# Kernel optimization log

Hardware: AMD Instinct MI355X
Metric: run time of the kernel (lower is better)

Reference implementation:

```python
import jax, jax.numpy as jnp
import numpy as np

B, N, DIM = 64, 197, 768        # batch, tokens (14*14 + cls), model dim
H, KD, D = 12, 64, 128          # heads, key_dim, v head dim (attn_ratio=2)
DH = H * D                      # 1536
HQKV = DH + 2 * H * KD          # 3072
EPS = 1e-5
SCALE = KD ** -0.5


def _bn(y, g, b):
    # BatchNorm1d in training mode over flattened (B*N, F): biased variance
    m = y.mean(axis=(0, 1))
    v = jnp.mean((y - m) ** 2, axis=(0, 1))
    return (y - m) * (g / jnp.sqrt(v + EPS)) + b


def setup_inputs() -> dict:
    key = jax.random.key(0)
    ks = jax.random.split(key, 7)
    return {
        "x": jax.random.normal(ks[0], (B, N, DIM), jnp.float32),
        "qkv_w": jax.random.normal(ks[1], (HQKV, DIM), jnp.float32) * 0.02,
        "qkv_g": 1.0 + 0.1 * jax.random.normal(ks[2], (HQKV,), jnp.float32),
        "qkv_b": 0.1 * jax.random.normal(ks[3], (HQKV,), jnp.float32),
        "proj_w": jax.random.normal(ks[4], (DIM, DH), jnp.float32) * 0.02,
        "proj_g": 1.0 + 0.1 * jax.random.normal(ks[5], (DIM,), jnp.float32),
        "proj_b": 0.1 * jax.random.normal(ks[6], (DIM,), jnp.float32),
    }


def reference(x, qkv_w, qkv_g, qkv_b, proj_w, proj_g, proj_b):
    # QKV projection: bias-free linear + train-mode BatchNorm1d
    qkv = _bn(jnp.einsum('bnc,fc->bnf', x, qkv_w), qkv_g, qkv_b)
    qkv = qkv.reshape(B, N, H, 2 * KD + D)
    q = qkv[..., :KD].transpose(0, 2, 1, 3)          # [B,H,N,KD]
    k = qkv[..., KD:2 * KD].transpose(0, 2, 1, 3)    # [B,H,N,KD]
    v = qkv[..., 2 * KD:].transpose(0, 2, 1, 3)      # [B,H,N,D]

    attn = jax.nn.softmax(jnp.einsum('bhqd,bhkd->bhqk', q, k) * SCALE, axis=-1)
    # auxiliary reduction: per-head-mean of cls-token row (global_attn update)
    cls_attn = attn[:, :, 0, 1:].mean(axis=1)        # [B, N-1]

    out = jnp.einsum('bhqk,bhkd->bhqd', attn, v)
    out = out.transpose(0, 2, 1, 3).reshape(B, N, DH)
    # proj: Hardswish activation, then linear + train-mode BatchNorm1d
    y = _bn(jnp.einsum('bnd,cd->bnc', jax.nn.hard_swish(out), proj_w), proj_g, proj_b)
    return y, cls_attn
```

## Files before the change

kernel.cpp:

```cpp
#include <hip/hip_runtime.h>
#include <hip/hip_bf16.h>

typedef __hip_bfloat16 bf16;
typedef __attribute__((ext_vector_type(4))) float f32x4;
typedef __attribute__((ext_vector_type(8))) short s16x8;
typedef __attribute__((ext_vector_type(4))) unsigned short u16x4;

#define NB 64
#define NT 197
#define DIM 768
#define NH 12
#define HQKV 3072
#define DH 1536
#define DV 128
#define MREAL (NB*NT)
#define MPAD 12800
#define KPAD 224
#define PSTR 232
#define CNT ((float)MREAL)

__device__ __forceinline__ float bf2f(bf16 v) { return __bfloat162float(v); }
__device__ __forceinline__ bf16  f2bf(float v){ return __float2bfloat16(v); }
__device__ __forceinline__ unsigned short f2bfu(float v){ return __builtin_bit_cast(unsigned short, __float2bfloat16(v)); }
__device__ __forceinline__ float u2f(unsigned short u){ return __builtin_bit_cast(float, (unsigned)u << 16); }

__device__ __forceinline__ void async16(const bf16* g, bf16* l) {
  __builtin_amdgcn_global_load_lds((const __attribute__((address_space(1))) void*)g,
                                   (__attribute__((address_space(3))) void*)l, 16, 0, 0);
}

__global__ void prep_kernel(const float* __restrict__ x, const float* __restrict__ qkv_w,
                            const float* __restrict__ proj_w,
                            bf16* __restrict__ xb, bf16* __restrict__ wqkvb,
                            bf16* __restrict__ wprojb, bf16* __restrict__ act,
                            bf16* __restrict__ vT,
                            float* __restrict__ statq, float* __restrict__ statp,
                            float* __restrict__ cls)
{
  const int stride = gridDim.x * blockDim.x;
  const int tid = blockIdx.x * blockDim.x + threadIdx.x;
  const u16x4 z4 = {0,0,0,0};
  for (int i = tid; i < MREAL*DIM/4; i += stride) {
    float4 v = ((const float4*)x)[i];
    u16x4 o = {f2bfu(v.x), f2bfu(v.y), f2bfu(v.z), f2bfu(v.w)};
    ((u16x4*)xb)[i] = o;
  }
  for (int i = tid; i < (MPAD-MREAL)*DIM/4; i += stride)
    ((u16x4*)(xb + (size_t)MREAL*DIM))[i] = z4;
  for (int i = tid; i < HQKV*DIM/4; i += stride) {
    float4 v = ((const float4*)qkv_w)[i];
    u16x4 o = {f2bfu(v.x), f2bfu(v.y), f2bfu(v.z), f2bfu(v.w)};
    ((u16x4*)wqkvb)[i] = o;
  }
  for (int i = tid; i < DIM*DH/4; i += stride) {
    float4 v = ((const float4*)proj_w)[i];
    u16x4 o = {f2bfu(v.x), f2bfu(v.y), f2bfu(v.z), f2bfu(v.w)};
    ((u16x4*)wprojb)[i] = o;
  }
  for (int i = tid; i < (MPAD-MREAL)*DH/4; i += stride)
    ((u16x4*)(act + (size_t)MREAL*DH))[i] = z4;
  for (int i = tid; i < NB*NH*DV*(KPAD-NT); i += stride) {
    int r = i / (KPAD-NT), c = NT + (i - r*(KPAD-NT));
    vT[(size_t)r*KPAD + c] = f2bf(0.f);
  }
  for (int i = tid; i < 2*HQKV; i += stride) statq[i] = 0.f;
  for (int i = tid; i < 2*DIM;  i += stride) statp[i] = 0.f;
  for (int i = tid; i < NB*(NT-1); i += stride) cls[i] = 0.f;
}

template<int K, int NT_TILES, bool VT, bool SWZ>
__global__ __launch_bounds__(256, 2)
void gemm64(const bf16* __restrict__ A, const bf16* __restrict__ Bw,
            bf16* __restrict__ C, bf16* __restrict__ vT,
            float* __restrict__ stats, int Ncols, int nblk)
{
  constexpr int NKT = K/64;
  __shared__ bf16 As[2][128*64];
  __shared__ bf16 Bs[2][128*64];
  int bid = blockIdx.x;
  if (SWZ) {
    const int q = nblk >> 3, r = nblk & 7;
    const int xcd = bid & 7, idx = bid >> 3;
    bid = (xcd < r ? xcd*(q+1) : r*(q+1) + (xcd-r)*q) + idx;
  }
  const int bn = bid % NT_TILES;
  const int bm = bid / NT_TILES;
  const int t = threadIdx.x;
  const int wave = t >> 6, lane = t & 63;
  const int wm = wave >> 1, wn = wave & 1;
  const int l15 = lane & 15, l4 = lane >> 4;

  const int sr = t >> 3;
  const int scol = ((t & 7) ^ (sr & 7)) * 8;
  const bf16* aG = A  + (size_t)(bm*128 + sr)*K + scol;
  const bf16* bG = Bw + (size_t)(bn*128 + sr)*K + scol;
  const int ldsOff = wave * 512;

  auto stage = [&](int slot, int kt) {
#pragma unroll
    for (int i = 0; i < 4; ++i) {
      async16(aG + kt*64 + (size_t)(i*32)*K, &As[slot][i*2048 + ldsOff]);
      async16(bG + kt*64 + (size_t)(i*32)*K, &Bs[slot][i*2048 + ldsOff]);
    }
  };

  f32x4 acc[4][4] = {};
  stage(0, 0);
  const int rswz = l15 & 7;
  for (int kt = 0; kt < NKT; ++kt) {
    if (kt + 1 < NKT) {
      stage((kt + 1) & 1, kt + 1);
      asm volatile("s_waitcnt vmcnt(8)" ::: "memory");
    } else {
      asm volatile("s_waitcnt vmcnt(0)" ::: "memory");
    }
    __builtin_amdgcn_s_barrier();
    asm volatile("" ::: "memory");

    const bf16* as = As[kt & 1];
    const bf16* bs = Bs[kt & 1];
#pragma unroll
    for (int ks = 0; ks < 2; ++ks) {
      s16x8 af[4], bfr[4];
#pragma unroll
      for (int i = 0; i < 4; ++i)
        af[i]  = *(const s16x8*)&as[(wm*64 + i*16 + l15)*64 + (((ks*4 + l4) ^ rswz)*8)];
#pragma unroll
      for (int i = 0; i < 4; ++i)
        bfr[i] = *(const s16x8*)&bs[(wn*64 + i*16 + l15)*64 + (((ks*4 + l4) ^ rswz)*8)];
      __builtin_amdgcn_s_setprio(1);
#pragma unroll
      for (int im = 0; im < 4; ++im)
#pragma unroll
        for (int in = 0; in < 4; ++in)
          acc[im][in] = __builtin_amdgcn_mfma_f32_16x16x32_bf16(af[im], bfr[in], acc[im][in], 0, 0, 0);
      __builtin_amdgcn_s_setprio(0);
    }
    asm volatile("" ::: "memory");
    __builtin_amdgcn_s_barrier();
    asm volatile("" ::: "memory");
  }

  const int gRow0 = bm*128 + wm*64;
  const int colBase = bn*128 + wn*64;
  if (!VT || (bn & 1) == 0) {
#pragma unroll
    for (int n = 0; n < 4; ++n) {
      const int col = colBase + n*16 + l15;
      float s = 0.f, sq = 0.f;
#pragma unroll
      for (int m = 0; m < 4; ++m) {
        const int r0 = gRow0 + m*16 + l4*4;
        const bool wr = r0 < MREAL;
#pragma unroll
        for (int j = 0; j < 4; ++j) {
          float v = acc[m][n][j];
          s += v; sq += v*v;
          if (wr) C[(size_t)(r0 + j)*Ncols + col] = f2bf(v);
        }
      }
      s  += __shfl_xor(s, 16);  s  += __shfl_xor(s, 32);
      sq += __shfl_xor(sq, 16); sq += __shfl_xor(sq, 32);
      if (l4 == 0) { atomicAdd(&stats[col], s); atomicAdd(&stats[Ncols + col], sq); }
    }
  } else {
    const int hh = bn >> 1;
#pragma unroll
    for (int n = 0; n < 4; ++n) {
      const int col = colBase + n*16 + l15;
      const int d = col & 127;
      float s = 0.f, sq = 0.f;
#pragma unroll
      for (int m = 0; m < 4; ++m) {
        const int r0 = gRow0 + m*16 + l4*4;
#pragma unroll
        for (int j = 0; j < 4; ++j) { float v = acc[m][n][j]; s += v; sq += v*v; }
        if (r0 < MREAL) {
          int b2 = r0 / 197;
          int n0 = r0 - b2*197;
          if (n0 <= NT-4) {
            bf16* dst = vT + ((size_t)((b2*NH + hh)*DV + d))*KPAD + n0;
#pragma unroll
            for (int j = 0; j < 4; ++j) dst[j] = f2bf(acc[m][n][j]);
          } else {
#pragma unroll
            for (int j = 0; j < 4; ++j) {
              int r = r0 + j; int b3 = r / 197; int nn = r - b3*197;
              vT[((size_t)((b3*NH + hh)*DV + d))*KPAD + nn] = f2bf(acc[m][n][j]);
            }
          }
        }
      }
      s  += __shfl_xor(s, 16);  s  += __shfl_xor(s, 32);
      sq += __shfl_xor(sq, 16); sq += __shfl_xor(sq, 32);
      if (l4 == 0) { atomicAdd(&stats[col], s); atomicAdd(&stats[Ncols + col], sq); }
    }
  }
}

template<int K, int NT_TILES, bool SWZ>
__global__ __launch_bounds__(256, 4)
void gemm32(const bf16* __restrict__ A, const bf16* __restrict__ Bw,
            bf16* __restrict__ C, float* __restrict__ stats, int Ncols, int nblk)
{
  constexpr int NKT = K/32;
  __shared__ bf16 As[2][128*32];
  __shared__ bf16 Bs[2][128*32];
  int bid = blockIdx.x;
  if (SWZ) {
    const int q = nblk >> 3, r = nblk & 7;
    const int xcd = bid & 7, idx = bid >> 3;
    bid = (xcd < r ? xcd*(q+1) : r*(q+1) + (xcd-r)*q) + idx;
  }
  const int bn = bid % NT_TILES;
  const int bm = bid / NT_TILES;
  const int t = threadIdx.x;
  const int wave = t >> 6, lane = t & 63;
  const int wm = wave >> 1, wn = wave & 1;
  const int l15 = lane & 15, l4 = lane >> 4;

  const int sr = t >> 2;
  const bf16* aG = A  + (size_t)(bm*128 + sr)*K + (t&3)*8;
  const bf16* bG = Bw + (size_t)(bn*128 + sr)*K + (t&3)*8;
  const int ldsOff = wave * 512;

  auto stage = [&](int slot, int kt) {
    async16(aG + kt*32,                &As[slot][ldsOff]);
    async16(aG + kt*32 + (size_t)64*K, &As[slot][ldsOff + 2048]);
    async16(bG + kt*32,                &Bs[slot][ldsOff]);
    async16(bG + kt*32 + (size_t)64*K, &Bs[slot][ldsOff + 2048]);
  };

  f32x4 acc[4][4] = {};
  stage(0, 0);
  for (int kt = 0; kt < NKT; ++kt) {
    if (kt + 1 < NKT) {
      stage((kt + 1) & 1, kt + 1);
      asm volatile("s_waitcnt vmcnt(4)" ::: "memory");
    } else {
      asm volatile("s_waitcnt vmcnt(0)" ::: "memory");
    }
    __builtin_amdgcn_s_barrier();
    asm volatile("" ::: "memory");

    const bf16* as = As[kt & 1];
    const bf16* bs = Bs[kt & 1];
    s16x8 af[4], bfr[4];
#pragma unroll
    for (int i = 0; i < 4; ++i) af[i]  = *(const s16x8*)&as[(wm*64 + i*16 + l15)*32 + l4*8];
#pragma unroll
    for (int i = 0; i < 4; ++i) bfr[i] = *(const s16x8*)&bs[(wn*64 + i*16 + l15)*32 + l4*8];
    __builtin_amdgcn_s_setprio(1);
#pragma unroll
    for (int im = 0; im < 4; ++im)
#pragma unroll
      for (int in = 0; in < 4; ++in)
        acc[im][in] = __builtin_amdgcn_mfma_f32_16x16x32_bf16(af[im], bfr[in], acc[im][in], 0, 0, 0);
    __builtin_amdgcn_s_setprio(0);
    asm volatile("" ::: "memory");
    __builtin_amdgcn_s_barrier();
    asm volatile("" ::: "memory");
  }

  const int gRow0 = bm*128 + wm*64;
  const int colBase = bn*128 + wn*64;
#pragma unroll
  for (int n = 0; n < 4; ++n) {
    const int col = colBase + n*16 + l15;
    float s = 0.f, sq = 0.f;
#pragma unroll
    for (int m = 0; m < 4; ++m) {
      const int r0 = gRow0 + m*16 + l4*4;
      const bool wr = r0 < MREAL;
#pragma unroll
      for (int j = 0; j < 4; ++j) {
        float v = acc[m][n][j];
        s += v; sq += v*v;
        if (wr) C[(size_t)(r0 + j)*Ncols + col] = f2bf(v);
      }
    }
    s  += __shfl_xor(s, 16);  s  += __shfl_xor(s, 32);
    sq += __shfl_xor(sq, 16); sq += __shfl_xor(sq, 32);
    if (l4 == 0) { atomicAdd(&stats[col], s); atomicAdd(&stats[Ncols + col], sq); }
  }
}

__global__ void finalize_stats(const float* __restrict__ stats, const float* __restrict__ g,
                               const float* __restrict__ bb, float* __restrict__ sb, int F,
                               float* __restrict__ qcw)
{
  int f = blockIdx.x * blockDim.x + threadIdx.x;
  if (f >= F) return;
  float m   = stats[f] / CNT;
  float var = stats[F + f] / CNT - m*m;
  float scl = g[f] / sqrtf(var + 1e-5f);
  float bia = bb[f] - m*scl;
  sb[f] = scl;
  sb[F + f] = bia;
  if (qcw && (f & 255) < 64) {
    float mk   = stats[f + 64] / CNT;
    float vark = stats[F + f + 64] / CNT - mk*mk;
    float sclk = g[f + 64] / sqrtf(vark + 1e-5f);
    int h = f >> 8, d = f & 63;
    qcw[h*128 + d]      = 0.125f * scl * sclk;
    qcw[h*128 + 64 + d] = 0.125f * bia * sclk;
  }
}

__global__ __launch_bounds__(512, 1)
void attn_kernel(const bf16* __restrict__ qkv, const bf16* __restrict__ vT,
                 const float* __restrict__ sb, const float* __restrict__ qcw,
                 bf16* __restrict__ act, float* __restrict__ cls)
{
  __shared__ bf16 k_lds[KPAD*64];
  __shared__ bf16 v_lds[DV*256];
  __shared__ bf16 p_all[8*16*PSTR];
  const int t = threadIdx.x;
  const int wave = t >> 6, lane = t & 63;
  const int l15 = lane & 15, l4 = lane >> 4;
  const int bh = blockIdx.x;
  const int b = bh / NH, h = bh - b*NH;
  const size_t rowBase = (size_t)b * NT;
  bf16* p_lds = &p_all[wave * (16*PSTR)];
  const bf16* Qp = qkv + rowBase*HQKV + h*256;
  const bf16* Kp = Qp + 64;
  const bf16* Vp = vT + (size_t)bh*DV*KPAD;
  const int fv = h*256 + 128;

  {
    const int ldsW = wave * 512;
#pragma unroll
    for (int p = 0; p < 4; ++p) {
      int lam = p*512 + t;
      if (lam < KPAD*8) {
        int row = lam >> 3, g = lam & 7;
        async16(Kp + (size_t)row*HQKV + ((g ^ (row & 7))*8), &k_lds[p*4096 + ldsW]);
      }
    }
#pragma unroll
    for (int p = 0; p < 8; ++p) {
      int lam = p*512 + t;
      int r = lam >> 5, sl = lam & 31;
      async16(Vp + (size_t)r*KPAD + ((sl ^ (r & 7))*8), &v_lds[p*4096 + ldsW]);
    }
  }
  __syncthreads();

  f32x4 c0a = *(const f32x4*)&qcw[h*128 + l4*8],      c0b = *(const f32x4*)&qcw[h*128 + l4*8 + 4];
  f32x4 w0a = *(const f32x4*)&qcw[h*128 + 64 + l4*8], w0b = *(const f32x4*)&qcw[h*128 + 64 + l4*8 + 4];
  f32x4 c1a = *(const f32x4*)&qcw[h*128 + 32 + l4*8], c1b = *(const f32x4*)&qcw[h*128 + 32 + l4*8 + 4];
  f32x4 w1a = *(const f32x4*)&qcw[h*128 + 96 + l4*8], w1b = *(const f32x4*)&qcw[h*128 + 96 + l4*8 + 4];

  const int kswz = l15 & 7;

  for (int ti = wave; ti < 13; ti += 8) {
    const int q0 = ti * 16;

    s16x8 aq0 = *(const s16x8*)&Qp[(size_t)(q0 + l15)*HQKV + l4*8];
    s16x8 aq1 = *(const s16x8*)&Qp[(size_t)(q0 + l15)*HQKV + 32 + l4*8];
    {
      s16x8 r0, r1;
#pragma unroll
      for (int j = 0; j < 4; ++j) {
        r0[j]   = (short)f2bfu(u2f((unsigned short)aq0[j])   * c0a[j] + w0a[j]);
        r0[j+4] = (short)f2bfu(u2f((unsigned short)aq0[j+4]) * c0b[j] + w0b[j]);
        r1[j]   = (short)f2bfu(u2f((unsigned short)aq1[j])   * c1a[j] + w1a[j]);
        r1[j+4] = (short)f2bfu(u2f((unsigned short)aq1[j+4]) * c1b[j] + w1b[j]);
      }
      aq0 = r0; aq1 = r1;
    }

    f32x4 scr[14];
#pragma unroll
    for (int kt = 0; kt < 14; ++kt) {
      const int krow = (kt*16 + l15)*64;
      s16x8 bk0 = *(const s16x8*)&k_lds[krow + ((l4 ^ kswz)*8)];
      s16x8 bk1 = *(const s16x8*)&k_lds[krow + (((4 + l4) ^ kswz)*8)];
      f32x4 z = {};
      z = __builtin_amdgcn_mfma_f32_16x16x32_bf16(aq0, bk0, z, 0, 0, 0);
      scr[kt] = __builtin_amdgcn_mfma_f32_16x16x32_bf16(aq1, bk1, z, 0, 0, 0);
    }

    float mx[4] = {-1e30f, -1e30f, -1e30f, -1e30f}, sm[4];
#pragma unroll
    for (int kt = 0; kt < 14; ++kt) {
      int colv = kt*16 + l15;
#pragma unroll
      for (int j = 0; j < 4; ++j) {
        if (colv >= NT) scr[kt][j] = -1e30f;
        mx[j] = fmaxf(mx[j], scr[kt][j]);
      }
    }
#pragma unroll
    for (int j = 0; j < 4; ++j) {
      mx[j] = fmaxf(mx[j], __shfl_xor(mx[j], 1));
      mx[j] = fmaxf(mx[j], __shfl_xor(mx[j], 2));
      mx[j] = fmaxf(mx[j], __shfl_xor(mx[j], 4));
      mx[j] = fmaxf(mx[j], __shfl_xor(mx[j], 8));
      sm[j] = 0.f;
    }
#pragma unroll
    for (int kt = 0; kt < 14; ++kt)
#pragma unroll
      for (int j = 0; j < 4; ++j) { float e = __expf(scr[kt][j] - mx[j]); scr[kt][j] = e; sm[j] += e; }
#pragma unroll
    for (int j = 0; j < 4; ++j) {
      sm[j] += __shfl_xor(sm[j], 1);
      sm[j] += __shfl_xor(sm[j], 2);
      sm[j] += __shfl_xor(sm[j], 4);
      sm[j] += __shfl_xor(sm[j], 8);
      sm[j] = 1.f / sm[j];
    }
    if (ti == 0 && l4 == 0) {
#pragma unroll
      for (int kt = 0; kt < 14; ++kt) {
        int colv = kt*16 + l15;
        if (colv >= 1 && colv < NT)
          atomicAdd(&cls[b*(NT-1) + colv - 1], scr[kt][0] * sm[0] * (1.f/NH));
      }
    }
#pragma unroll
    for (int kt = 0; kt < 14; ++kt) {
      int colv = kt*16 + l15;
#pragma unroll
      for (int j = 0; j < 4; ++j)
        p_lds[(l4*4 + j)*PSTR + colv] = f2bf(scr[kt][j] * sm[j]);
    }

    f32x4 ao[8] = {};
#pragma unroll
    for (int ks = 0; ks < 7; ++ks) {
      s16x8 ap = *(const s16x8*)&p_lds[l15*PSTR + ks*32 + l4*8];
#pragma unroll
      for (int dt = 0; dt < 8; ++dt) {
        const int vrow = (dt*16 + l15)*256;
        s16x8 bv = *(const s16x8*)&v_lds[vrow + (((ks*4 + l4) ^ kswz)*8)];
        ao[dt] = __builtin_amdgcn_mfma_f32_16x16x32_bf16(ap, bv, ao[dt], 0, 0, 0);
      }
    }
#pragma unroll
    for (int dt = 0; dt < 8; ++dt) {
      const int d = dt*16 + l15;
      const float av = sb[fv + d];
      const float bv = sb[HQKV + fv + d];
#pragma unroll
      for (int j = 0; j < 4; ++j) {
        int q = q0 + l4*4 + j;
        if (q < NT) {
          float v = ao[dt][j] * av + bv;
          float hs = v * fminf(fmaxf(v + 3.f, 0.f), 6.f) * (1.f/6.f);
          act[(rowBase + q)*DH + h*DV + d] = f2bf(hs);
        }
      }
    }
  }
}

__global__ void apply_bn(const bf16* __restrict__ y, const float* __restrict__ sb,
                         float* __restrict__ out)
{
  const int stride = gridDim.x * blockDim.x;
  for (int i = blockIdx.x * blockDim.x + threadIdx.x; i < MREAL*DIM/4; i += stride) {
    int c = (i*4) % DIM;
    u16x4 yv = *(const u16x4*)&y[(size_t)i*4];
    float4 o;
    o.x = u2f(yv.x) * sb[c]     + sb[DIM + c];
    o.y = u2f(yv.y) * sb[c + 1] + sb[DIM + c + 1];
    o.z = u2f(yv.z) * sb[c + 2] + sb[DIM + c + 2];
    o.w = u2f(yv.w) * sb[c + 3] + sb[DIM + c + 3];
    *(float4*)&out[(size_t)i*4] = o;
  }
}

extern "C" void kernel_launch(void* const* d_in, const int* in_sizes, int n_in,
                              void* d_out, int out_size, void* d_ws, size_t ws_size,
                              hipStream_t stream)
{
  const float* x      = (const float*)d_in[0];
  const float* qkv_w  = (const float*)d_in[1];
  const float* qkv_g  = (const float*)d_in[2];
  const float* qkv_b  = (const float*)d_in[3];
  const float* proj_w = (const float*)d_in[4];
  const float* proj_g = (const float*)d_in[5];
  const float* proj_b = (const float*)d_in[6];
  float* y_out   = (float*)d_out;
  float* cls_out = y_out + (size_t)MREAL * DIM;

  char* ws = (char*)d_ws;
  size_t off = 0;
  auto alloc = [&](size_t bytes) { void* p = ws + off; off += (bytes + 255) & ~(size_t)255; return p; };
  bf16* xb      = (bf16*)alloc((size_t)MPAD * DIM * 2);
  bf16* wqkvb   = (bf16*)alloc((size_t)HQKV * DIM * 2);
  bf16* wprojb  = (bf16*)alloc((size_t)DIM * DH * 2);
  bf16* qkv_raw = (bf16*)alloc((size_t)MPAD * HQKV * 2);
  bf16* act     = (bf16*)alloc((size_t)MPAD * DH * 2);
  bf16* y_raw   = (bf16*)alloc((size_t)MPAD * DIM * 2);
  bf16* vT      = (bf16*)alloc((size_t)NB * NH * DV * KPAD * 2);
  float* statq  = (float*)alloc((size_t)2 * HQKV * 4);
  float* sbq    = (float*)alloc((size_t)2 * HQKV * 4);
  float* statp  = (float*)alloc((size_t)2 * DIM * 4);
  float* sbp    = (float*)alloc((size_t)2 * DIM * 4);
  float* qcw    = (float*)alloc((size_t)NH * 128 * 4);

  prep_kernel<<<2048, 256, 0, stream>>>(x, qkv_w, proj_w, xb, wqkvb, wprojb, act, vT,
                                        statq, statp, cls_out);
  gemm64<DIM, HQKV/128, true, true><<<(MPAD/128)*(HQKV/128), 256, 0, stream>>>(
      xb, wqkvb, qkv_raw, vT, statq, HQKV, (MPAD/128)*(HQKV/128));
  finalize_stats<<<HQKV/256, 256, 0, stream>>>(statq, qkv_g, qkv_b, sbq, HQKV, qcw);
  attn_kernel<<<NB*NH, 512, 0, stream>>>(qkv_raw, vT, sbq, qcw, act, cls_out);
  gemm32<DH, DIM/128, true><<<(MPAD/128)*(DIM/128), 256, 0, stream>>>(
      act, wprojb, y_raw, statp, DIM, (MPAD/128)*(DIM/128));
  finalize_stats<<<DIM/256, 256, 0, stream>>>(statp, proj_g, proj_b, sbp, DIM, nullptr);
  apply_bn<<<2048, 256, 0, stream>>>(y_raw, sbp, y_out);
}
```

Measured before the change: 221.4 us.

## Enlarge QKV GEMM tile to 256x256 with 8 waves and grouped block order

```diff
diff --git a/kernel.cpp b/kernel.cpp
--- a/kernel.cpp
+++ b/kernel.cpp
@@ -69,42 +69,47 @@
 }
 
 template<int K, int NT_TILES, bool VT, bool SWZ>
-__global__ __launch_bounds__(256, 2)
-void gemm64(const bf16* __restrict__ A, const bf16* __restrict__ Bw,
-            bf16* __restrict__ C, bf16* __restrict__ vT,
-            float* __restrict__ stats, int Ncols, int nblk)
+__global__ __launch_bounds__(512, 1)
+void gemm256(const bf16* __restrict__ A, const bf16* __restrict__ Bw,
+             bf16* __restrict__ C, bf16* __restrict__ vT,
+             float* __restrict__ stats, int Ncols, int nblk)
 {
   constexpr int NKT = K/64;
-  __shared__ bf16 As[2][128*64];
-  __shared__ bf16 Bs[2][128*64];
+  __shared__ bf16 As[2][256*64];
+  __shared__ bf16 Bs[2][256*64];
   int bid = blockIdx.x;
   if (SWZ) {
     const int q = nblk >> 3, r = nblk & 7;
     const int xcd = bid & 7, idx = bid >> 3;
     bid = (xcd < r ? xcd*(q+1) : r*(q+1) + (xcd-r)*q) + idx;
   }
-  const int bn = bid % NT_TILES;
-  const int bm = bid / NT_TILES;
+  int bm, bn;
+  {
+    const int sup = bid / 30, w = bid % 30;
+    const int bmS = sup % 10, bnS = sup / 10;
+    bm = bmS*5 + w/6;
+    bn = bnS*6 + w%6;
+  }
   const int t = threadIdx.x;
   const int wave = t >> 6, lane = t & 63;
-  const int wm = wave >> 1, wn = wave & 1;
+  const int wr = wave >> 2, wc = wave & 3;
   const int l15 = lane & 15, l4 = lane >> 4;
 
   const int sr = t >> 3;
   const int scol = ((t & 7) ^ (sr & 7)) * 8;
-  const bf16* aG = A  + (size_t)(bm*128 + sr)*K + scol;
-  const bf16* bG = Bw + (size_t)(bn*128 + sr)*K + scol;
+  const bf16* aS = A  + (size_t)(bm*256 + sr)*K + scol;
+  const bf16* bS = Bw + (size_t)(bn*256 + sr)*K + scol;
   const int ldsOff = wave * 512;
 
   auto stage = [&](int slot, int kt) {
 #pragma unroll
     for (int i = 0; i < 4; ++i) {
-      async16(aG + kt*64 + (size_t)(i*32)*K, &As[slot][i*2048 + ldsOff]);
-      async16(bG + kt*64 + (size_t)(i*32)*K, &Bs[slot][i*2048 + ldsOff]);
+      async16(aS + kt*64 + (size_t)(i*64)*K, &As[slot][i*4096 + ldsOff]);
+      async16(bS + kt*64 + (size_t)(i*64)*K, &Bs[slot][i*4096 + ldsOff]);
     }
   };
 
-  f32x4 acc[4][4] = {};
+  f32x4 acc[8][4] = {};
   stage(0, 0);
   const int rswz = l15 & 7;
   for (int kt = 0; kt < NKT; ++kt) {
@@ -121,19 +126,20 @@
     const bf16* bs = Bs[kt & 1];
 #pragma unroll
     for (int ks = 0; ks < 2; ++ks) {
-      s16x8 af[4], bfr[4];
-#pragma unroll
-      for (int i = 0; i < 4; ++i)
-        af[i]  = *(const s16x8*)&as[(wm*64 + i*16 + l15)*64 + (((ks*4 + l4) ^ rswz)*8)];
-#pragma unroll
-      for (int i = 0; i < 4; ++i)
-        bfr[i] = *(const s16x8*)&bs[(wn*64 + i*16 + l15)*64 + (((ks*4 + l4) ^ rswz)*8)];
+      const int rg = ((ks*4 + l4) ^ rswz) * 8;
+      s16x8 af[8], bfr[4];
+#pragma unroll
+      for (int m = 0; m < 8; ++m)
+        af[m]  = *(const s16x8*)&as[(wr*128 + m*16 + l15)*64 + rg];
+#pragma unroll
+      for (int n = 0; n < 4; ++n)
+        bfr[n] = *(const s16x8*)&bs[(wc*64 + n*16 + l15)*64 + rg];
       __builtin_amdgcn_s_setprio(1);
 #pragma unroll
-      for (int im = 0; im < 4; ++im)
-#pragma unroll
-        for (int in = 0; in < 4; ++in)
-          acc[im][in] = __builtin_amdgcn_mfma_f32_16x16x32_bf16(af[im], bfr[in], acc[im][in], 0, 0, 0);
+      for (int m = 0; m < 8; ++m)
+#pragma unroll
+        for (int n = 0; n < 4; ++n)
+          acc[m][n] = __builtin_amdgcn_mfma_f32_16x16x32_bf16(af[m], bfr[n], acc[m][n], 0, 0, 0);
       __builtin_amdgcn_s_setprio(0);
     }
     asm volatile("" ::: "memory");
@@ -141,37 +147,28 @@
     asm volatile("" ::: "memory");
   }
 
-  const int gRow0 = bm*128 + wm*64;
-  const int colBase = bn*128 + wn*64;
-  if (!VT || (bn & 1) == 0) {
-#pragma unroll
-    for (int n = 0; n < 4; ++n) {
-      const int col = colBase + n*16 + l15;
-      float s = 0.f, sq = 0.f;
-#pragma unroll
-      for (int m = 0; m < 4; ++m) {
+  const int gRow0 = bm*256 + wr*128;
+  const int colBase = bn*256 + wc*64;
+#pragma unroll
+  for (int n = 0; n < 4; ++n) {
+    const int col = colBase + n*16 + l15;
+    float s = 0.f, sq = 0.f;
+    if (!VT || wc < 2) {
+#pragma unroll
+      for (int m = 0; m < 8; ++m) {
         const int r0 = gRow0 + m*16 + l4*4;
-        const bool wr = r0 < MREAL;
+        const bool wrk = r0 < MREAL;
 #pragma unroll
         for (int j = 0; j < 4; ++j) {
           float v = acc[m][n][j];
           s += v; sq += v*v;
-          if (wr) C[(size_t)(r0 + j)*Ncols + col] = f2bf(v);
+          if (wrk) C[(size_t)(r0 + j)*Ncols + col] = f2bf(v);
         }
       }
-      s  += __shfl_xor(s, 16);  s  += __shfl_xor(s, 32);
-      sq += __shfl_xor(sq, 16); sq += __shfl_xor(sq, 32);
-      if (l4 == 0) { atomicAdd(&stats[col], s); atomicAdd(&stats[Ncols + col], sq); }
-    }
-  } else {
-    const int hh = bn >> 1;
-#pragma unroll
-    for (int n = 0; n < 4; ++n) {
-      const int col = colBase + n*16 + l15;
-      const int d = col & 127;
-      float s = 0.f, sq = 0.f;
-#pragma unroll
-      for (int m = 0; m < 4; ++m) {
+    } else {
+      const int d = wc*64 + n*16 + l15 - 128;
+#pragma unroll
+      for (int m = 0; m < 8; ++m) {
         const int r0 = gRow0 + m*16 + l4*4;
 #pragma unroll
         for (int j = 0; j < 4; ++j) { float v = acc[m][n][j]; s += v; sq += v*v; }
@@ -179,22 +176,22 @@
           int b2 = r0 / 197;
           int n0 = r0 - b2*197;
           if (n0 <= NT-4) {
-            bf16* dst = vT + ((size_t)((b2*NH + hh)*DV + d))*KPAD + n0;
+            bf16* dst = vT + ((size_t)((b2*NH + bn)*DV + d))*KPAD + n0;
 #pragma unroll
             for (int j = 0; j < 4; ++j) dst[j] = f2bf(acc[m][n][j]);
           } else {
 #pragma unroll
             for (int j = 0; j < 4; ++j) {
               int r = r0 + j; int b3 = r / 197; int nn = r - b3*197;
-              vT[((size_t)((b3*NH + hh)*DV + d))*KPAD + nn] = f2bf(acc[m][n][j]);
+              vT[((size_t)((b3*NH + bn)*DV + d))*KPAD + nn] = f2bf(acc[m][n][j]);
             }
           }
         }
       }
-      s  += __shfl_xor(s, 16);  s  += __shfl_xor(s, 32);
-      sq += __shfl_xor(sq, 16); sq += __shfl_xor(sq, 32);
-      if (l4 == 0) { atomicAdd(&stats[col], s); atomicAdd(&stats[Ncols + col], sq); }
-    }
+    }
+    s  += __shfl_xor(s, 16);  s  += __shfl_xor(s, 32);
+    sq += __shfl_xor(sq, 16); sq += __shfl_xor(sq, 32);
+    if (l4 == 0) { atomicAdd(&stats[col], s); atomicAdd(&stats[Ncols + col], sq); }
   }
 }
 
@@ -504,8 +501,8 @@
 
   prep_kernel<<<2048, 256, 0, stream>>>(x, qkv_w, proj_w, xb, wqkvb, wprojb, act, vT,
                                         statq, statp, cls_out);
-  gemm64<DIM, HQKV/128, true, true><<<(MPAD/128)*(HQKV/128), 256, 0, stream>>>(
-      xb, wqkvb, qkv_raw, vT, statq, HQKV, (MPAD/128)*(HQKV/128));
+  gemm256<DIM, HQKV/256, true, true><<<(MPAD/256)*(HQKV/256), 512, 0, stream>>>(
+      xb, wqkvb, qkv_raw, vT, statq, HQKV, (MPAD/256)*(HQKV/256));
   finalize_stats<<<HQKV/256, 256, 0, stream>>>(statq, qkv_g, qkv_b, sbq, HQKV, qcw);
   attn_kernel<<<NB*NH, 512, 0, stream>>>(qkv_raw, vT, sbq, qcw, act, cls_out);
   gemm32<DH, DIM/128, true><<<(MPAD/128)*(DIM/128), 256, 0, stream>>>(
```

After: 224.7 us. About the same (+1.5%).
